# Kernel optimization log

Hardware: AMD Instinct MI355X
Metric: run time of the kernel (lower is better)

Reference implementation:

```python
import jax, jax.numpy as jnp
import numpy as np

D = 1152      # hidden_size
H = 16        # num_heads
K = D // H    # head_dim = 72
L = 2         # depth
I = 4304      # intermediate_size
M = 2         # spatial_merge_size
NPOS = 2304   # num_position_embeddings (48x48)
OUT = 2048    # out_hidden_size
CIN = 3 * 2 * 16 * 16  # C*tp*p*p = 1536
GRID = np.array([[1, 48, 48], [1, 32, 64], [2, 24, 40]], dtype=np.int32)


def _ln(x, s, b, eps=1e-6):
    mu = jnp.mean(x, -1, keepdims=True)
    var = jnp.mean((x - mu) ** 2, -1, keepdims=True)
    return (x - mu) * jax.lax.rsqrt(var + eps) * s + b


def _rot_half(x):
    h = x.shape[-1] // 2
    return jnp.concatenate([-x[..., h:], x[..., :h]], -1)


def _seg_bounds(g):
    b = [0]
    for t, h, w in g:
        for _ in range(int(t)):
            b.append(b[-1] + int(h) * int(w))
    return list(zip(b[:-1], b[1:]))


def _rope_cos_sin(g):
    half = K // 2  # rotary_half_dim
    max_hw = int(g[:, 1:].max())
    inv = 1.0 / (10000.0 ** (np.arange(0, half, 2, dtype=np.float64) / half))
    table = np.arange(max_hw)[:, None] * inv[None, :]  # (max_hw, half//2)
    pos = []
    for t, h, w in g:
        t, h, w = int(t), int(h), int(w)
        mh, mw = h // M, w // M
        row = np.broadcast_to(np.arange(mh)[:, None, None, None] * M + np.arange(M)[None, None, :, None], (mh, mw, M, M)).reshape(-1)
        col = np.broadcast_to(np.arange(mw)[None, :, None, None] * M + np.arange(M)[None, None, None, :], (mh, mw, M, M)).reshape(-1)
        c = np.stack([row, col], -1)
        if t > 1:
            c = np.tile(c, (t, 1))
        pos.append(c)
    pos = np.concatenate(pos, 0)
    emb = table[pos].reshape(pos.shape[0], -1)     # (N, half)
    emb = np.concatenate([emb, emb], -1)           # (N, head_dim)
    return jnp.asarray(np.cos(emb), jnp.float32), jnp.asarray(np.sin(emb), jnp.float32)


def _pos_embeds(pos_table, g):
    n = int(NPOS ** 0.5)
    outs = []
    for t, h, w in g:
        t, h, w = int(t), int(h), int(w)
        hi = np.linspace(0, n - 1, h); wi = np.linspace(0, n - 1, w)
        hf = np.floor(hi).astype(np.int32); wf = np.floor(wi).astype(np.int32)
        hc = np.clip(hf + 1, 0, n - 1); wc = np.clip(wf + 1, 0, n - 1)
        dh = (hi - hf).astype(np.float32); dw = (wi - wf).astype(np.float32)
        i00 = (hf[:, None] * n + wf[None, :]).reshape(-1)
        i01 = (hf[:, None] * n + wc[None, :]).reshape(-1)
        i10 = (hc[:, None] * n + wf[None, :]).reshape(-1)
        i11 = (hc[:, None] * n + wc[None, :]).reshape(-1)
        w00 = ((1 - dh)[:, None] * (1 - dw)[None, :]).reshape(-1, 1)
        w01 = ((1 - dh)[:, None] * dw[None, :]).reshape(-1, 1)
        w10 = (dh[:, None] * (1 - dw)[None, :]).reshape(-1, 1)
        w11 = (dh[:, None] * dw[None, :]).reshape(-1, 1)
        e = pos_table[i00] * w00 + pos_table[i01] * w01 + pos_table[i10] * w10 + pos_table[i11] * w11
        # spatial-merge reorder
        e = jnp.tile(e, (t, 1)).reshape(t, h // M, M, w // M, M, -1).transpose(0, 1, 3, 2, 4, 5).reshape(-1, D)
        outs.append(e)
    return jnp.concatenate(outs, 0)


def _forward(pixel_values, grid, patch_w, patch_b, pos_table, ln1_s, ln1_b, qkv_w, qkv_b,
             proj_w, proj_b, ln2_s, ln2_b, fc1_w, fc1_b, fc2_w, fc2_b,
             m_ln_s, m_ln_b, m_fc1_w, m_fc1_b, m_fc2_w, m_fc2_b):
    g = np.asarray(grid)
    # patch embed: conv with kernel==stride over whole patch == matmul on flattened patch
    x = pixel_values @ patch_w + patch_b               # (N, D)
    x = x + _pos_embeds(pos_table, g)
    cos, sin = _rope_cos_sin(g)                        # (N, K) each
    bounds = _seg_bounds(g)
    scale = K ** -0.5
    for l in range(L):
        h = _ln(x, ln1_s[l], ln1_b[l])
        N = h.shape[0]
        qkv = (h @ qkv_w[l] + qkv_b[l]).reshape(N, 3, H, K)
        q, k, v = qkv[:, 0], qkv[:, 1], qkv[:, 2]
        q = q * cos[:, None, :] + _rot_half(q) * sin[:, None, :]
        k = k * cos[:, None, :] + _rot_half(k) * sin[:, None, :]
        outs = []
        for s, e in bounds:  # static ragged segments (cu_seqlens)
            logits = jnp.einsum('lhk,mhk->hlm', q[s:e], k[s:e]) * scale
            wts = jax.nn.softmax(logits.astype(jnp.float32), -1).astype(logits.dtype)
            outs.append(jnp.einsum('hlm,mhk->lhk', wts, v[s:e]).reshape(e - s, H * K))
        attn = jnp.concatenate(outs, 0) @ proj_w[l] + proj_b[l]
        x = x + attn
        h2 = _ln(x, ln2_s[l], ln2_b[l])
        x = x + jax.nn.gelu(h2 @ fc1_w[l] + fc1_b[l], approximate=True) @ fc2_w[l] + fc2_b[l]
    normed = _ln(x, m_ln_s, m_ln_b).reshape(-1, D * M * M)
    return jax.nn.gelu(normed @ m_fc1_w + m_fc1_b, approximate=True) @ m_fc2_w + m_fc2_b


def setup_inputs() -> dict:
    key = jax.random.key(0)
    ks = jax.random.split(key, 16)
    def nrm(k, shp, s=0.02):
        return jax.random.normal(k, shp, jnp.float32) * s
    Ntok = int(sum(int(t) * int(h) * int(w) for t, h, w in GRID))  # 6272
    return {
        'pixel_values': nrm(ks[0], (Ntok, CIN), 1.0),
        'grid_thw': jnp.asarray(GRID),
        'patch_w': nrm(ks[1], (CIN, D)), 'patch_b': nrm(ks[2], (D,), 0.01),
        'pos_table': nrm(ks[3], (NPOS, D)),
        'ln1_s': jnp.ones((L, D)), 'ln1_b': jnp.zeros((L, D)),
        'qkv_w': nrm(ks[4], (L, D, 3 * D)), 'qkv_b': nrm(ks[5], (L, 3 * D), 0.01),
        'proj_w': nrm(ks[6], (L, D, D)), 'proj_b': nrm(ks[7], (L, D), 0.01),
        'ln2_s': jnp.ones((L, D)), 'ln2_b': jnp.zeros((L, D)),
        'fc1_w': nrm(ks[8], (L, D, I)), 'fc1_b': nrm(ks[9], (L, I), 0.01),
        'fc2_w': nrm(ks[10], (L, I, D)), 'fc2_b': nrm(ks[11], (L, D), 0.01),
        'm_ln_s': jnp.ones((D,)), 'm_ln_b': jnp.zeros((D,)),
        'm_fc1_w': nrm(ks[12], (D * M * M, D * M * M)), 'm_fc1_b': nrm(ks[13], (D * M * M,), 0.01),
        'm_fc2_w': nrm(ks[14], (D * M * M, OUT)), 'm_fc2_b': nrm(ks[15], (OUT,), 0.01),
    }


def reference(pixel_values, grid_thw, patch_w, patch_b, pos_table, ln1_s, ln1_b, qkv_w, qkv_b,
              proj_w, proj_b, ln2_s, ln2_b, fc1_w, fc1_b, fc2_w, fc2_b,
              m_ln_s, m_ln_b, m_fc1_w, m_fc1_b, m_fc2_w, m_fc2_b):
    return _forward(pixel_values, grid_thw, patch_w, patch_b, pos_table, ln1_s, ln1_b, qkv_w, qkv_b,
                    proj_w, proj_b, ln2_s, ln2_b, fc1_w, fc1_b, fc2_w, fc2_b,
                    m_ln_s, m_ln_b, m_fc1_w, m_fc1_b, m_fc2_w, m_fc2_b)
```

## Files before the change

### kernel.cpp

```cpp
#include <hip/hip_runtime.h>

typedef __bf16 bf16;
typedef float f32x4 __attribute__((ext_vector_type(4)));
typedef bf16 bf16x8 __attribute__((ext_vector_type(8)));

#define NTOK 6272
#define DMODEL 1152

__device__ __forceinline__ void tok_geo(int t, int& row, int& col, int& gh, int& gw) {
    int local;
    if (t < 2304)      { local = t;        gh = 48; gw = 48; }
    else if (t < 4352) { local = t - 2304; gh = 32; gw = 64; }
    else if (t < 5312) { local = t - 4352; gh = 24; gw = 40; }
    else               { local = t - 5312; gh = 24; gw = 40; }
    int mc = local & 1;
    int mr = (local >> 1) & 1;
    int rest = local >> 2;
    int mwc = gw >> 1;
    int mw = rest % mwc;
    int mh = rest / mwc;
    row = mh * 2 + mr;
    col = mw * 2 + mc;
}

__device__ __forceinline__ float gelu_tanh(float v) {
    float c = v + 0.044715f * v * v * v;
    return 0.5f * v * (1.0f + tanhf(0.7978845608028654f * c));
}

__global__ void detect_kernel(const unsigned short* __restrict__ px, int* __restrict__ flag) {
    int tid = threadIdx.x;
    int cnt = 0;
    for (int i = tid * 8; i < tid * 8 + 8; i++) {
        unsigned e = (px[i] >> 7) & 0xFF;
        if (e < 100u || e > 140u) cnt++;
    }
#pragma unroll
    for (int off = 32; off > 0; off >>= 1) cnt += __shfl_down(cnt, off);
    if (tid == 0) *flag = (cnt > 64) ? 1 : 0;
}

template <typename T>
__device__ __forceinline__ void load8(const T* src, bf16* dst, bool pred) {
    if (!pred) {
        uint4 z = {0, 0, 0, 0};
        *(uint4*)dst = z;
        return;
    }
    if constexpr (sizeof(T) == 2) {
        *(uint4*)dst = *(const uint4*)src;
    } else {
        float4 a = *(const float4*)src;
        float4 b = *(const float4*)(src + 4);
        dst[0] = (bf16)a.x; dst[1] = (bf16)a.y; dst[2] = (bf16)a.z; dst[3] = (bf16)a.w;
        dst[4] = (bf16)b.x; dst[5] = (bf16)b.y; dst[6] = (bf16)b.z; dst[7] = (bf16)b.w;
    }
}

template <typename TI>
__global__ __launch_bounds__(256) void pos_embed_kernel(const int* __restrict__ flag,
                                                        const TI* __restrict__ tab,
                                                        bf16* __restrict__ x) {
    if (*flag != (sizeof(TI) == 4 ? 1 : 0)) return;
    int t = blockIdx.x;
    int row, col, gh, gw;
    tok_geo(t, row, col, gh, gw);
    float hi = row * 47.0f / (gh - 1);
    float wi = col * 47.0f / (gw - 1);
    int hf = (int)hi, wf = (int)wi;
    int hc = min(hf + 1, 47), wc = min(wf + 1, 47);
    float dh = hi - hf, dw = wi - wf;
    float w00 = (1.f - dh) * (1.f - dw);
    float w01 = (1.f - dh) * dw;
    float w10 = dh * (1.f - dw);
    float w11 = dh * dw;
    const TI* p00 = tab + (size_t)(hf * 48 + wf) * DMODEL;
    const TI* p01 = tab + (size_t)(hf * 48 + wc) * DMODEL;
    const TI* p10 = tab + (size_t)(hc * 48 + wf) * DMODEL;
    const TI* p11 = tab + (size_t)(hc * 48 + wc) * DMODEL;
    bf16* xr = x + (size_t)t * DMODEL;
    for (int d = threadIdx.x; d < DMODEL; d += 256)
        xr[d] = (bf16)(w00 * (float)p00[d] + w01 * (float)p01[d] +
                       w10 * (float)p10[d] + w11 * (float)p11[d]);
}

template <typename TI>
__global__ __launch_bounds__(256) void ln_kernel(const int* __restrict__ flag,
                                                 const bf16* __restrict__ x,
                                                 const TI* __restrict__ s,
                                                 const TI* __restrict__ b,
                                                 bf16* __restrict__ out) {
    if (*flag != (sizeof(TI) == 4 ? 1 : 0)) return;
    const int row = blockIdx.x;
    const int tid = threadIdx.x;
    __shared__ float red[4];
    const bf16* xr = x + (size_t)row * DMODEL;
    float vals[5];
    int cnt = 0;
    float sum = 0.f;
    for (int i = tid; i < DMODEL; i += 256) { vals[cnt] = (float)xr[i]; sum += vals[cnt]; cnt++; }
#pragma unroll
    for (int off = 32; off > 0; off >>= 1) sum += __shfl_down(sum, off);
    if ((tid & 63) == 0) red[tid >> 6] = sum;
    __syncthreads();
    float mean = (red[0] + red[1] + red[2] + red[3]) * (1.0f / DMODEL);
    float vs = 0.f;
    for (int i = 0; i < cnt; i++) { float d = vals[i] - mean; vs += d * d; }
#pragma unroll
    for (int off = 32; off > 0; off >>= 1) vs += __shfl_down(vs, off);
    __syncthreads();
    if ((tid & 63) == 0) red[tid >> 6] = vs;
    __syncthreads();
    float var = (red[0] + red[1] + red[2] + red[3]) * (1.0f / DMODEL);
    float inv = rsqrtf(var + 1e-6f);
    int idx = 0;
    for (int i = tid; i < DMODEL; i += 256)
        out[(size_t)row * DMODEL + i] = (bf16)((vals[idx++] - mean) * inv * (float)s[i] + (float)b[i]);
}

__global__ __launch_bounds__(256) void rope_inplace_kernel(bf16* __restrict__ qkv) {
    int idx = blockIdx.x * 256 + threadIdx.x;
    const int total = NTOK * 16 * 36;
    if (idx >= total) return;
    int j = idx % 36;
    int rest = idx / 36;
    int h = rest & 15;
    int t = rest >> 4;
    bf16* base = qkv + (size_t)t * 3456 + h * 72;
    int row, col, gh, gw;
    tok_geo(t, row, col, gh, gw);
    float pos = (float)((j < 18) ? row : col);
    int fi = (j < 18) ? j : j - 18;
    float ang = pos * powf(10000.0f, -(float)fi / 18.0f);
    float cv = cosf(ang), sv = sinf(ang);
    float q0v = (float)base[j],        q1v = (float)base[j + 36];
    float k0v = (float)base[1152 + j], k1v = (float)base[1152 + j + 36];
    base[j]          = (bf16)(q0v * cv - q1v * sv);
    base[j + 36]     = (bf16)(q1v * cv + q0v * sv);
    base[1152 + j]      = (bf16)(k0v * cv - k1v * sv);
    base[1152 + j + 36] = (bf16)(k1v * cv + k0v * sv);
}

__global__ __launch_bounds__(256) void attn_kernel(const bf16* __restrict__ qkv,
                                                   bf16* __restrict__ outp) {
    const int bx = blockIdx.x;
    const int head = bx & 15;
    const int qt = bx >> 4;
    int sbase, slen, qtb;
    if (qt < 36)      { sbase = 0;    slen = 2304; qtb = 0;  }
    else if (qt < 68) { sbase = 2304; slen = 2048; qtb = 36; }
    else if (qt < 83) { sbase = 4352; slen = 960;  qtb = 68; }
    else              { sbase = 5312; slen = 960;  qtb = 83; }
    const int q0 = sbase + (qt - qtb) * 64;

    __shared__ bf16 Qs[64][104];
    __shared__ bf16 Ks[64][104];
    __shared__ bf16 Vs[80][72];
    __shared__ bf16 Ps[64][72];

    const int tid = threadIdx.x;
    const int wv = tid >> 6;
    const int lane = tid & 63;
    const int quad = lane >> 4;
    const int l15 = lane & 15;

    const size_t hoff = (size_t)head * 72;

    for (int c = tid; c < 768; c += 256) {
        int r = c / 12, cc = (c % 12) * 8;
        uint4 v = {0, 0, 0, 0};
        if (cc < 72) v = *(const uint4*)(qkv + (size_t)(q0 + r) * 3456 + hoff + cc);
        *(uint4*)&Qs[r][cc] = v;
    }

    f32x4 o[5] = {};
    float m_i[4], l_i[4];
#pragma unroll
    for (int r = 0; r < 4; r++) { m_i[r] = -1e30f; l_i[r] = 0.f; }

    const float scale = 0.117851130197758f;
    const int nkv = slen >> 6;
    for (int kt = 0; kt < nkv; kt++) {
        const int k0 = sbase + kt * 64;
        __syncthreads();
        for (int c = tid; c < 768; c += 256) {
            int r = c / 12, cc = (c % 12) * 8;
            uint4 v = {0, 0, 0, 0};
            if (cc < 72) v = *(const uint4*)(qkv + (size_t)(k0 + r) * 3456 + 1152 + hoff + cc);
            *(uint4*)&Ks[r][cc] = v;
        }
        for (int c = tid; c < 576; c += 256) {
            int r = c & 63, cc = (c >> 6) * 8;
            uint4 v = *(const uint4*)(qkv + (size_t)(k0 + r) * 3456 + 2304 + hoff + cc);
            const bf16* e = (const bf16*)&v;
#pragma unroll
            for (int i = 0; i < 8; i++) Vs[cc + i][r] = e[i];
        }
        for (int c = tid; c < 64; c += 256) {
            int r = 72 + (c >> 3), cc = (c & 7) * 8;
            uint4 z = {0, 0, 0, 0};
            *(uint4*)&Vs[r][cc] = z;
        }
        __syncthreads();

        f32x4 sfr[4] = {};
#pragma unroll
        for (int kc = 0; kc < 96; kc += 32) {
            bf16x8 aq = *(const bf16x8*)&Qs[wv * 16 + l15][kc + quad * 8];
#pragma unroll
            for (int nt = 0; nt < 4; nt++) {
                bf16x8 bk = *(const bf16x8*)&Ks[nt * 16 + l15][kc + quad * 8];
                sfr[nt] = __builtin_amdgcn_mfma_f32_16x16x32_bf16(aq, bk, sfr[nt], 0, 0, 0);
            }
        }
#pragma unroll
        for (int nt = 0; nt < 4; nt++)
#pragma unroll
            for (int reg = 0; reg < 4; reg++) sfr[nt][reg] *= scale;

        float alpha[4], rs[4];
#pragma unroll
        for (int reg = 0; reg < 4; reg++) {
            float mx = fmaxf(fmaxf(sfr[0][reg], sfr[1][reg]), fmaxf(sfr[2][reg], sfr[3][reg]));
            mx = fmaxf(mx, __shfl_xor(mx, 1));
            mx = fmaxf(mx, __shfl_xor(mx, 2));
            mx = fmaxf(mx, __shfl_xor(mx, 4));
            mx = fmaxf(mx, __shfl_xor(mx, 8));
            float mn = fmaxf(m_i[reg], mx);
            alpha[reg] = __expf(m_i[reg] - mn);
            m_i[reg] = mn;
            rs[reg] = 0.f;
        }
#pragma unroll
        for (int nt = 0; nt < 4; nt++)
#pragma unroll
            for (int reg = 0; reg < 4; reg++) {
                float p = __expf(sfr[nt][reg] - m_i[reg]);
                sfr[nt][reg] = p;
                rs[reg] += p;
            }
#pragma unroll
        for (int reg = 0; reg < 4; reg++) {
            float r = rs[reg];
            r += __shfl_xor(r, 1);
            r += __shfl_xor(r, 2);
            r += __shfl_xor(r, 4);
            r += __shfl_xor(r, 8);
            l_i[reg] = l_i[reg] * alpha[reg] + r;
        }
#pragma unroll
        for (int nt = 0; nt < 5; nt++)
#pragma unroll
            for (int reg = 0; reg < 4; reg++) o[nt][reg] *= alpha[reg];

#pragma unroll
        for (int nt = 0; nt < 4; nt++)
#pragma unroll
            for (int reg = 0; reg < 4; reg++)
                Ps[wv * 16 + quad * 4 + reg][nt * 16 + l15] = (bf16)sfr[nt][reg];
        __syncthreads();

#pragma unroll
        for (int kc = 0; kc < 64; kc += 32) {
            bf16x8 ap = *(const bf16x8*)&Ps[wv * 16 + l15][kc + quad * 8];
#pragma unroll
            for (int nt = 0; nt < 5; nt++) {
                bf16x8 bv = *(const bf16x8*)&Vs[nt * 16 + l15][kc + quad * 8];
                o[nt] = __builtin_amdgcn_mfma_f32_16x16x32_bf16(ap, bv, o[nt], 0, 0, 0);
            }
        }
    }

#pragma unroll
    for (int nt = 0; nt < 5; nt++)
#pragma unroll
        for (int reg = 0; reg < 4; reg++) {
            int c = nt * 16 + l15;
            if (c < 72) {
                int tok = q0 + wv * 16 + quad * 4 + reg;
                outp[(size_t)tok * DMODEL + head * 72 + c] = (bf16)(o[nt][reg] / l_i[reg]);
            }
        }
}

template <int MODE, typename TA, typename TB>
__global__ __launch_bounds__(256) void gemm_kernel(const int* __restrict__ flag,
                                                   const TA* __restrict__ A,
                                                   const TB* __restrict__ B,
                                                   const TB* __restrict__ bias,
                                                   void* __restrict__ outp,
                                                   int M, int N, int K) {
    if (*flag != (sizeof(TB) == 4 ? 1 : 0)) return;
    __shared__ bf16 As[128][40];
    __shared__ bf16 Bs[128][40];
    const int tid = threadIdx.x;
    const int m0 = blockIdx.y * 128;
    const int n0 = blockIdx.x * 128;
    const int wv = tid >> 6;
    const int lane = tid & 63;
    const int quad = lane >> 4;
    const int l15 = lane & 15;
    const int wr = (wv >> 1) * 64;
    const int wc = (wv & 1) * 64;

    const int a_row = tid >> 1;
    const int a_col = (tid & 1) * 16;
    const int b_k = tid & 31;
    const int b_n = (tid >> 5) * 16;

    f32x4 acc[4][4] = {};

    for (int k0 = 0; k0 < K; k0 += 32) {
        __syncthreads();
        {
            bf16 ea[16];
            int gr = m0 + a_row;
            const TA* ap = A + (size_t)gr * K + k0 + a_col;
            load8(ap, ea, gr < M && (k0 + a_col) < K);
            load8(ap + 8, ea + 8, gr < M && (k0 + a_col + 8) < K);
            *(uint4*)&As[a_row][a_col] = *(uint4*)ea;
            *(uint4*)&As[a_row][a_col + 8] = *(uint4*)(ea + 8);
        }
        {
            bf16 eb[16];
            int gk = k0 + b_k;
            const TB* bp = B + (size_t)gk * N + n0 + b_n;
            load8(bp, eb, gk < K && (n0 + b_n) < N);
            load8(bp + 8, eb + 8, gk < K && (n0 + b_n + 8) < N);
#pragma unroll
            for (int i = 0; i < 16; i++) Bs[b_n + i][b_k] = eb[i];
        }
        __syncthreads();

        bf16x8 af[4], bfv[4];
#pragma unroll
        for (int mi = 0; mi < 4; mi++) af[mi] = *(const bf16x8*)&As[wr + mi * 16 + l15][quad * 8];
#pragma unroll
        for (int ni = 0; ni < 4; ni++) bfv[ni] = *(const bf16x8*)&Bs[wc + ni * 16 + l15][quad * 8];
#pragma unroll
        for (int mi = 0; mi < 4; mi++)
#pragma unroll
            for (int ni = 0; ni < 4; ni++)
                acc[mi][ni] = __builtin_amdgcn_mfma_f32_16x16x32_bf16(af[mi], bfv[ni], acc[mi][ni], 0, 0, 0);
    }

#pragma unroll
    for (int mi = 0; mi < 4; mi++) {
#pragma unroll
        for (int ni = 0; ni < 4; ni++) {
#pragma unroll
            for (int reg = 0; reg < 4; reg++) {
                int r = m0 + wr + mi * 16 + quad * 4 + reg;
                int c = n0 + wc + ni * 16 + l15;
                if (r < M && c < N) {
                    float v = acc[mi][ni][reg] + (float)bias[c];
                    if (MODE == 1) v = gelu_tanh(v);
                    if (MODE == 2) {
                        bf16* o = (bf16*)outp;
                        size_t idx = (size_t)r * N + c;
                        o[idx] = (bf16)((float)o[idx] + v);
                    } else if (MODE == 3) {
                        TB* o = (TB*)outp;
                        o[(size_t)r * N + c] = (TB)v;
                    } else {
                        bf16* o = (bf16*)outp;
                        o[(size_t)r * N + c] = (bf16)v;
                    }
                }
            }
        }
    }
}


template <typename TI>
__global__ __launch_bounds__(256) void cvt_kernel(const int* __restrict__ flag,
                                                  const TI* __restrict__ in,
                                                  bf16* __restrict__ out, int n8) {
    if (*flag != (sizeof(TI) == 4 ? 1 : 0)) return;
    for (int i = blockIdx.x * 256 + threadIdx.x; i < n8; i += gridDim.x * 256) {
        bf16 e[8];
        load8(in + (size_t)i * 8, e, true);
        *(uint4*)(out + (size_t)i * 8) = *(uint4*)e;
    }
}

template <typename TI>
__global__ __launch_bounds__(256) void transpose_w_kernel(const int* __restrict__ flag,
                                                          const TI* __restrict__ B,
                                                          bf16* __restrict__ T,
                                                          int K, int N, int Kpad) {
    if (*flag != (sizeof(TI) == 4 ? 1 : 0)) return;
    __shared__ bf16 t[64][72];
    const int k0 = blockIdx.y * 64, n0 = blockIdx.x * 64;
    const int tid = threadIdx.x;
    const int kk = tid >> 2;
    const int nn0 = (tid & 3) * 16;
    bf16 e[16];
    bool ok = (k0 + kk < K) && (n0 + nn0 < N);
    const TI* src = B + (size_t)(k0 + kk) * N + n0 + nn0;
    load8(src, e, ok);
    load8(src + 8, e + 8, ok);
#pragma unroll
    for (int i = 0; i < 16; i++) t[nn0 + i][kk] = e[i];
    __syncthreads();
    const int nn = tid >> 2;
    const int j16 = (tid & 3) * 16;
    if (n0 + nn < N && k0 + j16 < Kpad) {
        bf16* dst = T + (size_t)(n0 + nn) * Kpad + k0 + j16;
        *(uint4*)dst = *(uint4*)&t[nn][j16];
        *(uint4*)(dst + 8) = *(uint4*)&t[nn][j16 + 8];
    }
}

template <typename TI>
__global__ __launch_bounds__(256) void cvt_bias_kernel(const int* __restrict__ flag,
        const TI* p0, const TI* p1, const TI* p2, const TI* p3, const TI* p4,
        const TI* p5, const TI* p6, const TI* p7, const TI* p8, const TI* p9,
        const TI* p10, bf16* __restrict__ out) {
    if (*flag != (sizeof(TI) == 4 ? 1 : 0)) return;
    const int lens[11] = {1152, 3456, 3456, 1152, 1152, 4304, 4304, 1152, 1152, 4608, 2048};
    const int offs[11] = {0, 1152, 4608, 8064, 9216, 10368, 14672, 18976, 20128, 21280, 25888};
    int b = blockIdx.x;
    const TI* src = (b == 0) ? p0 : (b == 1) ? p1 : (b == 2) ? p2 : (b == 3) ? p3
                  : (b == 4) ? p4 : (b == 5) ? p5 : (b == 6) ? p6 : (b == 7) ? p7
                  : (b == 8) ? p8 : (b == 9) ? p9 : p10;
    for (int i = threadIdx.x; i < lens[b]; i += 256) out[offs[b] + i] = (bf16)(float)src[i];
}

typedef const __attribute__((address_space(1))) void* gas_ptr;
typedef __attribute__((address_space(3))) void* las_ptr;
__device__ __forceinline__ void gload16(const bf16* g, bf16* l) {
    __builtin_amdgcn_global_load_lds((gas_ptr)g, (las_ptr)l, 16, 0, 0);
}

template <int MODE>
__global__ __launch_bounds__(256) void gemm_lds_kernel(const int* __restrict__ flag,
        const bf16* __restrict__ A, const bf16* __restrict__ BT,
        const bf16* __restrict__ bias, void* __restrict__ outp,
        int M, int N, int K, int ldc) {
    __shared__ bf16 As[128][32];
    __shared__ bf16 Bs[128][32];
    const int tid = threadIdx.x;
    const int m0 = blockIdx.y * 128;
    const int n0 = blockIdx.x * 128;
    const int wv = tid >> 6;
    const int lane = tid & 63;
    const int quad = lane >> 4;
    const int l15 = lane & 15;
    const int wr = (wv >> 1) * 64;
    const int wc = (wv & 1) * 64;

    const int sr = wv * 32 + (lane >> 2);
    const int sc = (lane & 3) * 8;
    const bf16* aP0 = A + (size_t)min(m0 + sr, M - 1) * K + sc;
    const bf16* aP1 = A + (size_t)min(m0 + sr + 16, M - 1) * K + sc;
    const bf16* bP0 = BT + (size_t)min(n0 + sr, N - 1) * K + sc;
    const bf16* bP1 = BT + (size_t)min(n0 + sr + 16, N - 1) * K + sc;
    bf16* lA0 = &As[wv * 32][0];
    bf16* lA1 = &As[wv * 32 + 16][0];
    bf16* lB0 = &Bs[wv * 32][0];
    bf16* lB1 = &Bs[wv * 32 + 16][0];

    f32x4 acc[4][4] = {};
    for (int k0 = 0; k0 < K; k0 += 32) {
        __syncthreads();
        gload16(aP0 + k0, lA0);
        gload16(aP1 + k0, lA1);
        gload16(bP0 + k0, lB0);
        gload16(bP1 + k0, lB1);
        __syncthreads();
        bf16x8 af[4], bfv[4];
#pragma unroll
        for (int mi = 0; mi < 4; mi++) af[mi] = *(const bf16x8*)&As[wr + mi * 16 + l15][quad * 8];
#pragma unroll
        for (int ni = 0; ni < 4; ni++) bfv[ni] = *(const bf16x8*)&Bs[wc + ni * 16 + l15][quad * 8];
#pragma unroll
        for (int mi = 0; mi < 4; mi++)
#pragma unroll
            for (int ni = 0; ni < 4; ni++)
                acc[mi][ni] = __builtin_amdgcn_mfma_f32_16x16x32_bf16(af[mi], bfv[ni], acc[mi][ni], 0, 0, 0);
    }

    const int isf32 = (MODE == 3) ? *flag : 0;
#pragma unroll
    for (int mi = 0; mi < 4; mi++) {
#pragma unroll
        for (int ni = 0; ni < 4; ni++) {
#pragma unroll
            for (int reg = 0; reg < 4; reg++) {
                int r = m0 + wr + mi * 16 + quad * 4 + reg;
                int c = n0 + wc + ni * 16 + l15;
                if (r < M && c < ldc) {
                    float v = 0.f;
                    if (c < N) {
                        v = acc[mi][ni][reg] + (float)bias[c];
                        if (MODE == 1) v = gelu_tanh(v);
                    }
                    if (MODE == 2) {
                        bf16* o = (bf16*)outp;
                        size_t idx = (size_t)r * ldc + c;
                        o[idx] = (bf16)((float)o[idx] + v);
                    } else if (MODE == 3) {
                        if (isf32) ((float*)outp)[(size_t)r * ldc + c] = v;
                        else       ((bf16*)outp)[(size_t)r * ldc + c] = (bf16)v;
                    } else {
                        ((bf16*)outp)[(size_t)r * ldc + c] = (bf16)v;
                    }
                }
            }
        }
    }
}

#define OFF_PATCH  0ULL
#define OFF_QKV    1769472ULL
#define QKV_SZ     3981312ULL
#define OFF_PROJ   9732096ULL
#define PROJ_SZ    1327104ULL
#define OFF_FC1    12386304ULL
#define FC1_SZ     4958208ULL
#define OFF_FC2    22302720ULL
#define FC2_SZ     4976640ULL
#define OFF_MFC1   32256000ULL
#define OFF_MFC2   53489664ULL
#define OFF_BIAS   62926848ULL
#define WS_NEEDED  209001280ULL

extern "C" void kernel_launch(void* const* d_in, const int* in_sizes, int n_in,
                              void* d_out, int out_size, void* d_ws, size_t ws_size,
                              hipStream_t stream) {
    char* ws = (char*)d_ws;
    int* flag  = (int*)ws;
    bf16* x    = (bf16*)(ws + 256);
    bf16* h    = (bf16*)(ws + 256 + 14450688);
    bf16* bufA = (bf16*)(ws + 256 + 28901376);

    detect_kernel<<<1, 64, 0, stream>>>((const unsigned short*)d_in[0], flag);

    if (ws_size >= WS_NEEDED) {
        bf16* wT = (bf16*)(ws + 256 + 28901376 + 54190080);
        bf16* bias = wT + OFF_BIAS;
        bf16* px = bufA;

        cvt_kernel<bf16><<<1024, 256, 0, stream>>>(flag, (const bf16*)d_in[0], px, 1204224);
        cvt_kernel<float><<<1024, 256, 0, stream>>>(flag, (const float*)d_in[0], px, 1204224);

        auto T2 = [&](const void* srcBase, size_t eoff, bf16* dst, int K, int N, int Kpad) {
            dim3 g((N + 63) / 64, (Kpad + 63) / 64);
            transpose_w_kernel<bf16><<<g, 256, 0, stream>>>(flag, (const bf16*)srcBase + eoff, dst, K, N, Kpad);
            transpose_w_kernel<float><<<g, 256, 0, stream>>>(flag, (const float*)srcBase + eoff, dst, K, N, Kpad);
        };
        T2(d_in[2], 0, wT + OFF_PATCH, 1536, 1152, 1536);
        for (int l = 0; l < 2; l++) {
            T2(d_in[7],  (size_t)l * 1152 * 3456, wT + OFF_QKV + l * QKV_SZ, 1152, 3456, 1152);
            T2(d_in[9],  (size_t)l * 1152 * 1152, wT + OFF_PROJ + l * PROJ_SZ, 1152, 1152, 1152);
            T2(d_in[13], (size_t)l * 1152 * 4304, wT + OFF_FC1 + l * FC1_SZ, 1152, 4304, 1152);
            T2(d_in[15], (size_t)l * 4304 * 1152, wT + OFF_FC2 + l * FC2_SZ, 4304, 1152, 4320);
        }
        T2(d_in[19], 0, wT + OFF_MFC1, 4608, 4608, 4608);
        T2(d_in[21], 0, wT + OFF_MFC2, 4608, 2048, 4608);

        cvt_bias_kernel<bf16><<<11, 256, 0, stream>>>(flag,
            (const bf16*)d_in[3],
            (const bf16*)d_in[8], (const bf16*)d_in[8] + 3456,
            (const bf16*)d_in[10], (const bf16*)d_in[10] + 1152,
            (const bf16*)d_in[14], (const bf16*)d_in[14] + 4304,
            (const bf16*)d_in[16], (const bf16*)d_in[16] + 1152,
            (const bf16*)d_in[20], (const bf16*)d_in[22], bias);
        cvt_bias_kernel<float><<<11, 256, 0, stream>>>(flag,
            (const float*)d_in[3],
            (const float*)d_in[8], (const float*)d_in[8] + 3456,
            (const float*)d_in[10], (const float*)d_in[10] + 1152,
            (const float*)d_in[14], (const float*)d_in[14] + 4304,
            (const float*)d_in[16], (const float*)d_in[16] + 1152,
            (const float*)d_in[20], (const float*)d_in[22], bias);

        pos_embed_kernel<bf16><<<NTOK, 256, 0, stream>>>(flag, (const bf16*)d_in[4], x);
        pos_embed_kernel<float><<<NTOK, 256, 0, stream>>>(flag, (const float*)d_in[4], x);

        gemm_lds_kernel<2><<<dim3(9, 49), 256, 0, stream>>>(flag, px, wT + OFF_PATCH,
                                                            bias + 0, x, NTOK, 1152, 1536, 1152);

        for (int l = 0; l < 2; l++) {
            ln_kernel<bf16><<<NTOK, 256, 0, stream>>>(flag, x, (const bf16*)d_in[5] + l * 1152,
                                                      (const bf16*)d_in[6] + l * 1152, h);
            ln_kernel<float><<<NTOK, 256, 0, stream>>>(flag, x, (const float*)d_in[5] + l * 1152,
                                                       (const float*)d_in[6] + l * 1152, h);
            gemm_lds_kernel<0><<<dim3(27, 49), 256, 0, stream>>>(flag, h, wT + OFF_QKV + l * QKV_SZ,
                                                                 bias + 1152 + l * 3456, bufA,
                                                                 NTOK, 3456, 1152, 3456);
            rope_inplace_kernel<<<(NTOK * 16 * 36 + 255) / 256, 256, 0, stream>>>(bufA);
            attn_kernel<<<98 * 16, 256, 0, stream>>>(bufA, h);
            gemm_lds_kernel<2><<<dim3(9, 49), 256, 0, stream>>>(flag, h, wT + OFF_PROJ + l * PROJ_SZ,
                                                                bias + 8064 + l * 1152, x,
                                                                NTOK, 1152, 1152, 1152);
            ln_kernel<bf16><<<NTOK, 256, 0, stream>>>(flag, x, (const bf16*)d_in[11] + l * 1152,
                                                      (const bf16*)d_in[12] + l * 1152, h);
            ln_kernel<float><<<NTOK, 256, 0, stream>>>(flag, x, (const float*)d_in[11] + l * 1152,
                                                       (const float*)d_in[12] + l * 1152, h);
            gemm_lds_kernel<1><<<dim3(34, 49), 256, 0, stream>>>(flag, h, wT + OFF_FC1 + l * FC1_SZ,
                                                                 bias + 10368 + l * 4304, bufA,
                                                                 NTOK, 4304, 1152, 4320);
            gemm_lds_kernel<2><<<dim3(9, 49), 256, 0, stream>>>(flag, bufA, wT + OFF_FC2 + l * FC2_SZ,
                                                                bias + 18976 + l * 1152, x,
                                                                NTOK, 1152, 4320, 1152);
        }
        ln_kernel<bf16><<<NTOK, 256, 0, stream>>>(flag, x, (const bf16*)d_in[17], (const bf16*)d_in[18], h);
        ln_kernel<float><<<NTOK, 256, 0, stream>>>(flag, x, (const float*)d_in[17], (const float*)d_in[18], h);
        gemm_lds_kernel<1><<<dim3(36, 13), 256, 0, stream>>>(flag, h, wT + OFF_MFC1,
                                                             bias + 21280, bufA, 1568, 4608, 4608, 4608);
        gemm_lds_kernel<3><<<dim3(16, 13), 256, 0, stream>>>(flag, bufA, wT + OFF_MFC2,
                                                             bias + 25888, d_out, 1568, 2048, 4608, 2048);
        return;
    }

    {
        pos_embed_kernel<bf16><<<NTOK, 256, 0, stream>>>(flag, (const bf16*)d_in[4], x);
        pos_embed_kernel<float><<<NTOK, 256, 0, stream>>>(flag, (const float*)d_in[4], x);
        gemm_kernel<2, bf16, bf16><<<dim3(9, 49), 256, 0, stream>>>(
            flag, (const bf16*)d_in[0], (const bf16*)d_in[2], (const bf16*)d_in[3], x, NTOK, 1152, 1536);
        gemm_kernel<2, float, float><<<dim3(9, 49), 256, 0, stream>>>(
            flag, (const float*)d_in[0], (const float*)d_in[2], (const float*)d_in[3], x, NTOK, 1152, 1536);
    }
    for (int l = 0; l < 2; l++) {
        ln_kernel<bf16><<<NTOK, 256, 0, stream>>>(flag, x, (const bf16*)d_in[5] + l * 1152,
                                                  (const bf16*)d_in[6] + l * 1152, h);
        ln_kernel<float><<<NTOK, 256, 0, stream>>>(flag, x, (const float*)d_in[5] + l * 1152,
                                                   (const float*)d_in[6] + l * 1152, h);
        gemm_kernel<0, bf16, bf16><<<dim3(27, 49), 256, 0, stream>>>(
            flag, h, (const bf16*)d_in[7] + (size_t)l * 1152 * 3456,
            (const bf16*)d_in[8] + l * 3456, bufA, NTOK, 3456, 1152);
        gemm_kernel<0, bf16, float><<<dim3(27, 49), 256, 0, stream>>>(
            flag, h, (const float*)d_in[7] + (size_t)l * 1152 * 3456,
            (const float*)d_in[8] + l * 3456, bufA, NTOK, 3456, 1152);
        rope_inplace_kernel<<<(NTOK * 16 * 36 + 255) / 256, 256, 0, stream>>>(bufA);
        attn_kernel<<<98 * 16, 256, 0, stream>>>(bufA, h);
        gemm_kernel<2, bf16, bf16><<<dim3(9, 49), 256, 0, stream>>>(
            flag, h, (const bf16*)d_in[9] + (size_t)l * 1152 * 1152,
            (const bf16*)d_in[10] + l * 1152, x, NTOK, 1152, 1152);
        gemm_kernel<2, bf16, float><<<dim3(9, 49), 256, 0, stream>>>(
            flag, h, (const float*)d_in[9] + (size_t)l * 1152 * 1152,
            (const float*)d_in[10] + l * 1152, x, NTOK, 1152, 1152);
        ln_kernel<bf16><<<NTOK, 256, 0, stream>>>(flag, x, (const bf16*)d_in[11] + l * 1152,
                                                  (const bf16*)d_in[12] + l * 1152, h);
        ln_kernel<float><<<NTOK, 256, 0, stream>>>(flag, x, (const float*)d_in[11] + l * 1152,
                                                   (const float*)d_in[12] + l * 1152, h);
        gemm_kernel<1, bf16, bf16><<<dim3(34, 49), 256, 0, stream>>>(
            flag, h, (const bf16*)d_in[13] + (size_t)l * 1152 * 4304,
            (const bf16*)d_in[14] + l * 4304, bufA, NTOK, 4304, 1152);
        gemm_kernel<1, bf16, float><<<dim3(34, 49), 256, 0, stream>>>(
            flag, h, (const float*)d_in[13] + (size_t)l * 1152 * 4304,
            (const float*)d_in[14] + l * 4304, bufA, NTOK, 4304, 1152);
        gemm_kernel<2, bf16, bf16><<<dim3(9, 49), 256, 0, stream>>>(
            flag, bufA, (const bf16*)d_in[15] + (size_t)l * 4304 * 1152,
            (const bf16*)d_in[16] + l * 1152, x, NTOK, 1152, 4304);
        gemm_kernel<2, bf16, float><<<dim3(9, 49), 256, 0, stream>>>(
            flag, bufA, (const float*)d_in[15] + (size_t)l * 4304 * 1152,
            (const float*)d_in[16] + l * 1152, x, NTOK, 1152, 4304);
    }
    ln_kernel<bf16><<<NTOK, 256, 0, stream>>>(flag, x, (const bf16*)d_in[17], (const bf16*)d_in[18], h);
    ln_kernel<float><<<NTOK, 256, 0, stream>>>(flag, x, (const float*)d_in[17], (const float*)d_in[18], h);
    gemm_kernel<1, bf16, bf16><<<dim3(36, 13), 256, 0, stream>>>(
        flag, h, (const bf16*)d_in[19], (const bf16*)d_in[20], bufA, 1568, 4608, 4608);
    gemm_kernel<1, bf16, float><<<dim3(36, 13), 256, 0, stream>>>(
        flag, h, (const float*)d_in[19], (const float*)d_in[20], bufA, 1568, 4608, 4608);
    gemm_kernel<3, bf16, bf16><<<dim3(16, 13), 256, 0, stream>>>(
        flag, bufA, (const bf16*)d_in[21], (const bf16*)d_in[22], d_out, 1568, 2048, 4608);
    gemm_kernel<3, bf16, float><<<dim3(16, 13), 256, 0, stream>>>(
        flag, bufA, (const float*)d_in[21], (const float*)d_in[22], d_out, 1568, 2048, 4608);
}
```

Measured before the change: 2.297 ms.

## Pipeline attention K/V loads through registers and streamline softmax rescaling

The attention kernel now keeps Q in registers instead of a shared tile and prefetches the next K/V tile into registers while computing the current one. It also switches to exp2 with a folded scale constant and skips the rescale of the accumulator when no row maximum grows. It removes the barrier before the P·V step, which is safe because each wave only reads its own rows of Ps. Occupancy is requested with a launch bound of 4 blocks. These changes aim to hide global load latency and cut ALU and shared-memory work, at the cost of extra register pressure.

```diff
diff --git a/kernel.cpp b/kernel.cpp
--- a/kernel.cpp
+++ b/kernel.cpp
@@ -141,8 +141,8 @@
     base[1152 + j + 36] = (bf16)(k1v * cv + k0v * sv);
 }
 
-__global__ __launch_bounds__(256) void attn_kernel(const bf16* __restrict__ qkv,
-                                                   bf16* __restrict__ outp) {
+__global__ __launch_bounds__(256, 4) void attn_kernel(const bf16* __restrict__ qkv,
+                                                      bf16* __restrict__ outp) {
     const int bx = blockIdx.x;
     const int head = bx & 15;
     const int qt = bx >> 4;
@@ -153,7 +153,6 @@
     else              { sbase = 5312; slen = 960;  qtb = 83; }
     const int q0 = sbase + (qt - qtb) * 64;
 
-    __shared__ bf16 Qs[64][104];
     __shared__ bf16 Ks[64][104];
     __shared__ bf16 Vs[80][72];
     __shared__ bf16 Ps[64][72];
@@ -166,76 +165,131 @@
 
     const size_t hoff = (size_t)head * 72;
 
+    for (int c = tid; c < 64; c += 256) {
+        int r = 72 + (c >> 3), cc = (c & 7) * 8;
+        uint4 z = {0, 0, 0, 0};
+        *(uint4*)&Vs[r][cc] = z;
+    }
+
     for (int c = tid; c < 768; c += 256) {
         int r = c / 12, cc = (c % 12) * 8;
         uint4 v = {0, 0, 0, 0};
         if (cc < 72) v = *(const uint4*)(qkv + (size_t)(q0 + r) * 3456 + hoff + cc);
-        *(uint4*)&Qs[r][cc] = v;
-    }
+        *(uint4*)&Ks[r][cc] = v;
+    }
+    __syncthreads();
+    bf16x8 aq[3];
+#pragma unroll
+    for (int i = 0; i < 3; i++) aq[i] = *(const bf16x8*)&Ks[wv * 16 + l15][i * 32 + quad * 8];
+
+    int k_r[3], k_c[3];
+    bool kvalid[3];
+    const bf16* kp[3];
+#pragma unroll
+    for (int j = 0; j < 3; j++) {
+        int c = tid + 256 * j;
+        k_r[j] = c / 12;
+        k_c[j] = (c % 12) * 8;
+        kvalid[j] = k_c[j] < 72;
+        kp[j] = qkv + (size_t)(sbase + k_r[j]) * 3456 + 1152 + hoff + k_c[j];
+    }
+    int v_r[3], v_c[3];
+    const bf16* vp[3];
+#pragma unroll
+    for (int j = 0; j < 3; j++) {
+        int c = tid + 256 * j;
+        v_r[j] = c & 63;
+        v_c[j] = (c >> 6) * 8;
+        vp[j] = qkv + (size_t)(sbase + v_r[j]) * 3456 + 2304 + hoff + v_c[j];
+    }
+    const bool v2ok = tid < 64;
+    const int stepE = 64 * 3456;
+
+    uint4 kreg[3], vreg[3];
+    const uint4 z4 = {0, 0, 0, 0};
+#pragma unroll
+    for (int j = 0; j < 3; j++) {
+        kreg[j] = kvalid[j] ? *(const uint4*)kp[j] : z4;
+        if (kvalid[j]) kp[j] += stepE;
+    }
+    vreg[0] = *(const uint4*)vp[0]; vp[0] += stepE;
+    vreg[1] = *(const uint4*)vp[1]; vp[1] += stepE;
+    vreg[2] = v2ok ? *(const uint4*)vp[2] : z4;
+    if (v2ok) vp[2] += stepE;
 
     f32x4 o[5] = {};
     float m_i[4], l_i[4];
 #pragma unroll
     for (int r = 0; r < 4; r++) { m_i[r] = -1e30f; l_i[r] = 0.f; }
 
-    const float scale = 0.117851130197758f;
+    const float C1 = 0.17002234f;
     const int nkv = slen >> 6;
     for (int kt = 0; kt < nkv; kt++) {
-        const int k0 = sbase + kt * 64;
         __syncthreads();
-        for (int c = tid; c < 768; c += 256) {
-            int r = c / 12, cc = (c % 12) * 8;
-            uint4 v = {0, 0, 0, 0};
-            if (cc < 72) v = *(const uint4*)(qkv + (size_t)(k0 + r) * 3456 + 1152 + hoff + cc);
-            *(uint4*)&Ks[r][cc] = v;
-        }
-        for (int c = tid; c < 576; c += 256) {
-            int r = c & 63, cc = (c >> 6) * 8;
-            uint4 v = *(const uint4*)(qkv + (size_t)(k0 + r) * 3456 + 2304 + hoff + cc);
-            const bf16* e = (const bf16*)&v;
-#pragma unroll
-            for (int i = 0; i < 8; i++) Vs[cc + i][r] = e[i];
-        }
-        for (int c = tid; c < 64; c += 256) {
-            int r = 72 + (c >> 3), cc = (c & 7) * 8;
-            uint4 z = {0, 0, 0, 0};
-            *(uint4*)&Vs[r][cc] = z;
+#pragma unroll
+        for (int j = 0; j < 3; j++) *(uint4*)&Ks[k_r[j]][k_c[j]] = kreg[j];
+#pragma unroll
+        for (int j = 0; j < 2; j++) {
+            const bf16* e = (const bf16*)&vreg[j];
+#pragma unroll
+            for (int i = 0; i < 8; i++) Vs[v_c[j] + i][v_r[j]] = e[i];
+        }
+        if (v2ok) {
+            const bf16* e = (const bf16*)&vreg[2];
+#pragma unroll
+            for (int i = 0; i < 8; i++) Vs[64 + i][v_r[2]] = e[i];
         }
         __syncthreads();
 
+        if (kt + 1 < nkv) {
+#pragma unroll
+            for (int j = 0; j < 3; j++)
+                if (kvalid[j]) { kreg[j] = *(const uint4*)kp[j]; kp[j] += stepE; }
+            vreg[0] = *(const uint4*)vp[0]; vp[0] += stepE;
+            vreg[1] = *(const uint4*)vp[1]; vp[1] += stepE;
+            if (v2ok) { vreg[2] = *(const uint4*)vp[2]; vp[2] += stepE; }
+        }
+
         f32x4 sfr[4] = {};
 #pragma unroll
-        for (int kc = 0; kc < 96; kc += 32) {
-            bf16x8 aq = *(const bf16x8*)&Qs[wv * 16 + l15][kc + quad * 8];
+        for (int kc = 0; kc < 3; kc++)
 #pragma unroll
             for (int nt = 0; nt < 4; nt++) {
-                bf16x8 bk = *(const bf16x8*)&Ks[nt * 16 + l15][kc + quad * 8];
-                sfr[nt] = __builtin_amdgcn_mfma_f32_16x16x32_bf16(aq, bk, sfr[nt], 0, 0, 0);
+                bf16x8 bk = *(const bf16x8*)&Ks[nt * 16 + l15][kc * 32 + quad * 8];
+                sfr[nt] = __builtin_amdgcn_mfma_f32_16x16x32_bf16(aq[kc], bk, sfr[nt], 0, 0, 0);
             }
-        }
+
+        float mx[4];
+#pragma unroll
+        for (int reg = 0; reg < 4; reg++) {
+            float m = fmaxf(fmaxf(sfr[0][reg], sfr[1][reg]), fmaxf(sfr[2][reg], sfr[3][reg]));
+            m = fmaxf(m, __shfl_xor(m, 1));
+            m = fmaxf(m, __shfl_xor(m, 2));
+            m = fmaxf(m, __shfl_xor(m, 4));
+            m = fmaxf(m, __shfl_xor(m, 8));
+            mx[reg] = m;
+        }
+        bool grow = (mx[0] > m_i[0]) || (mx[1] > m_i[1]) || (mx[2] > m_i[2]) || (mx[3] > m_i[3]);
+        if (__any(grow)) {
+#pragma unroll
+            for (int reg = 0; reg < 4; reg++) {
+                float mn = fmaxf(m_i[reg], mx[reg]);
+                float a = __builtin_amdgcn_exp2f((m_i[reg] - mn) * C1);
+                m_i[reg] = mn;
+                l_i[reg] *= a;
+#pragma unroll
+                for (int nt = 0; nt < 5; nt++) o[nt][reg] *= a;
+            }
+        }
+        float mc[4];
+#pragma unroll
+        for (int reg = 0; reg < 4; reg++) mc[reg] = m_i[reg] * C1;
+        float rs[4] = {0.f, 0.f, 0.f, 0.f};
 #pragma unroll
         for (int nt = 0; nt < 4; nt++)
 #pragma unroll
-            for (int reg = 0; reg < 4; reg++) sfr[nt][reg] *= scale;
-
-        float alpha[4], rs[4];
-#pragma unroll
-        for (int reg = 0; reg < 4; reg++) {
-            float mx = fmaxf(fmaxf(sfr[0][reg], sfr[1][reg]), fmaxf(sfr[2][reg], sfr[3][reg]));
-            mx = fmaxf(mx, __shfl_xor(mx, 1));
-            mx = fmaxf(mx, __shfl_xor(mx, 2));
-            mx = fmaxf(mx, __shfl_xor(mx, 4));
-            mx = fmaxf(mx, __shfl_xor(mx, 8));
-            float mn = fmaxf(m_i[reg], mx);
-            alpha[reg] = __expf(m_i[reg] - mn);
-            m_i[reg] = mn;
-            rs[reg] = 0.f;
-        }
-#pragma unroll
-        for (int nt = 0; nt < 4; nt++)
-#pragma unroll
             for (int reg = 0; reg < 4; reg++) {
-                float p = __expf(sfr[nt][reg] - m_i[reg]);
+                float p = __builtin_amdgcn_exp2f(fmaf(sfr[nt][reg], C1, -mc[reg]));
                 sfr[nt][reg] = p;
                 rs[reg] += p;
             }
@@ -246,26 +300,21 @@
             r += __shfl_xor(r, 2);
             r += __shfl_xor(r, 4);
             r += __shfl_xor(r, 8);
-            l_i[reg] = l_i[reg] * alpha[reg] + r;
-        }
-#pragma unroll
-        for (int nt = 0; nt < 5; nt++)
-#pragma unroll
-            for (int reg = 0; reg < 4; reg++) o[nt][reg] *= alpha[reg];
+            l_i[reg] += r;
+        }
 
 #pragma unroll
         for (int nt = 0; nt < 4; nt++)
 #pragma unroll
             for (int reg = 0; reg < 4; reg++)
                 Ps[wv * 16 + quad * 4 + reg][nt * 16 + l15] = (bf16)sfr[nt][reg];
-        __syncthreads();
-
-#pragma unroll
-        for (int kc = 0; kc < 64; kc += 32) {
-            bf16x8 ap = *(const bf16x8*)&Ps[wv * 16 + l15][kc + quad * 8];
+
+#pragma unroll
+        for (int kc = 0; kc < 2; kc++) {
+            bf16x8 ap = *(const bf16x8*)&Ps[wv * 16 + l15][kc * 32 + quad * 8];
 #pragma unroll
             for (int nt = 0; nt < 5; nt++) {
-                bf16x8 bv = *(const bf16x8*)&Vs[nt * 16 + l15][kc + quad * 8];
+                bf16x8 bv = *(const bf16x8*)&Vs[nt * 16 + l15][kc * 32 + quad * 8];
                 o[nt] = __builtin_amdgcn_mfma_f32_16x16x32_bf16(ap, bv, o[nt], 0, 0, 0);
             }
         }
```

After: 2.342 ms. About the same (+2.0%).
